# Kernel tuning notes

Hardware: AMD Instinct MI355X
Metric: run time of the kernel (lower is better)

Reference implementation:

```python
import jax, jax.numpy as jnp
from jax import lax
import numpy as np

REG = 0.1  # regularization_strength
EPS = 1e-12  # F.normalize clamp


def pav_nonincreasing(y):
    """Pool-Adjacent-Violators: argmin_v ||v - y||^2 s.t. v_1 >= v_2 >= ... >= v_n.
    Stack-based O(n) sweep, jit-compatible (fixed shapes)."""
    n = y.shape[0]
    sums0 = jnp.zeros(n, y.dtype)
    cnts0 = jnp.zeros(n, y.dtype)

    def body(i, state):
        sums, cnts, ptr = state
        cur_s = y[i]
        cur_c = jnp.asarray(1.0, y.dtype)

        def cond(c):
            cs, cc, p, sm, ct = c
            j = jnp.maximum(p - 1, 0)
            # merge while prev block mean < current mean (violates nonincreasing)
            return (p > 0) & (sm[j] * cc < cs * ct[j])

        def merge(c):
            cs, cc, p, sm, ct = c
            return (cs + sm[p - 1], cc + ct[p - 1], p - 1, sm, ct)

        cs, cc, p, sums, cnts = lax.while_loop(cond, merge, (cur_s, cur_c, ptr, sums, cnts))
        sums = sums.at[p].set(cs)
        cnts = cnts.at[p].set(cc)
        return (sums, cnts, p + 1)

    sums, cnts, ptr = lax.fori_loop(0, n, body, (sums0, cnts0, jnp.int32(0)))
    means = sums / jnp.maximum(cnts, 1)
    bounds = jnp.cumsum(cnts)  # block end positions; bounds[ptr-1] == n, stale tail harmless
    bid = jnp.searchsorted(bounds, jnp.arange(n, dtype=y.dtype) + 0.5)
    return means[bid]


def soft_rank_desc_row(values):
    """fast-soft-sort soft_rank, direction='DESCENDING', regularization='l2'.
    Projection of values*scale onto permutahedron(n..1) via isotonic regression."""
    n = values.shape[0]
    scale = -1.0 / REG  # DESCENDING => sign = -1
    z = values * scale
    perm = jnp.argsort(-z)           # sort z descending
    s = z[perm]
    w = jnp.arange(n, 0, -1, dtype=values.dtype)  # n, n-1, ..., 1
    dual = pav_nonincreasing(s - w)
    primal = s - dual
    inv = jnp.argsort(perm)
    return primal[inv]


def setup_inputs() -> dict:
    key = jax.random.key(0)
    kq, kc = jax.random.split(key)
    query_embed = jax.random.normal(kq, (16, 384), dtype=jnp.float32)
    corpus_embeds = jax.random.normal(kc, (50000, 384), dtype=jnp.float32)
    return {"query_embed": query_embed, "corpus_embeds": corpus_embeds, "k": 100}


def reference(query_embed, corpus_embeds, k):
    q = query_embed / jnp.maximum(
        jnp.linalg.norm(query_embed, axis=-1, keepdims=True), EPS)
    c = corpus_embeds / jnp.maximum(
        jnp.linalg.norm(corpus_embeds, axis=-1, keepdims=True), EPS)
    similarities = q @ c.T  # (batch, num_docs) cosine sims
    soft_ranks = jax.vmap(soft_rank_desc_row)(similarities)
    return similarities, soft_ranks
```

## Files before the change

### kernel.cpp

```cpp
#include <hip/hip_runtime.h>
#include <hip/hip_bf16.h>

#define NQ 16
#define DIM 384
#define KSTEPS (DIM / 32)
#define SUMS_STRIDE 16

typedef __attribute__((ext_vector_type(8))) short bf16x8;
typedef __attribute__((ext_vector_type(4))) float f32x4;

__global__ __launch_bounds__(128) void norm_q_kernel(
    const float* __restrict__ q, __hip_bfloat16* __restrict__ qbf,
    float* __restrict__ sums) {
  int b = blockIdx.x, t = threadIdx.x;
  float ss = 0.f;
  for (int k = t; k < DIM; k += 128) {
    float x = q[b * DIM + k];
    ss += x * x;
  }
  #pragma unroll
  for (int o = 32; o > 0; o >>= 1) ss += __shfl_down(ss, o, 64);
  __shared__ float wsum[2];
  if ((t & 63) == 0) wsum[t >> 6] = ss;
  __syncthreads();
  float inv = 1.0f / fmaxf(sqrtf(wsum[0] + wsum[1]), 1e-12f);
  for (int k = t; k < DIM; k += 128)
    qbf[b * DIM + k] = __float2bfloat16(q[b * DIM + k] * inv);
  if (b == 0 && t < NQ) sums[t * SUMS_STRIDE] = 0.f;
}

__global__ __launch_bounds__(256, 3) void sim_mfma_kernel(
    const float* __restrict__ corpus, const __hip_bfloat16* __restrict__ qbf,
    float* __restrict__ out_sims, float* __restrict__ sums, int n) {
  int lane = threadIdx.x & 63;
  int wid = threadIdx.x >> 6;
  int col = lane & 15;
  int quad = lane >> 4;
  int doc = blockIdx.x * 64 + wid * 16 + col;
  int dload = doc < n ? doc : n - 1;

  bf16x8 afrag[KSTEPS];
  const __hip_bfloat16* qrow = qbf + col * DIM + quad * 8;
  #pragma unroll
  for (int ks = 0; ks < KSTEPS; ++ks)
    afrag[ks] = *reinterpret_cast<const bf16x8*>(qrow + ks * 32);

  const float4* crow =
      reinterpret_cast<const float4*>(corpus + (size_t)dload * DIM + quad * 8);
  float4 v[2 * KSTEPS];
  #pragma unroll
  for (int ks = 0; ks < KSTEPS; ++ks) {
    v[2 * ks] = crow[ks * 8];
    v[2 * ks + 1] = crow[ks * 8 + 1];
  }

  f32x4 acc = {0.f, 0.f, 0.f, 0.f};
  float nrm2 = 0.f;
  #pragma unroll
  for (int ks = 0; ks < KSTEPS; ++ks) {
    float4 v0 = v[2 * ks], v1 = v[2 * ks + 1];
    nrm2 += v0.x * v0.x + v0.y * v0.y + v0.z * v0.z + v0.w * v0.w +
            v1.x * v1.x + v1.y * v1.y + v1.z * v1.z + v1.w * v1.w;
    union { bf16x8 b; __hip_bfloat162 h[4]; } u;
    u.h[0] = __float22bfloat162_rn(float2{v0.x, v0.y});
    u.h[1] = __float22bfloat162_rn(float2{v0.z, v0.w});
    u.h[2] = __float22bfloat162_rn(float2{v1.x, v1.y});
    u.h[3] = __float22bfloat162_rn(float2{v1.z, v1.w});
    acc = __builtin_amdgcn_mfma_f32_16x16x32_bf16(afrag[ks], u.b, acc, 0, 0, 0);
  }

  nrm2 += __shfl_xor(nrm2, 16, 64);
  nrm2 += __shfl_xor(nrm2, 32, 64);
  float inv = 1.0f / fmaxf(sqrtf(nrm2), 1e-12f);

  bool valid = doc < n;
  float vv[4];
  #pragma unroll
  for (int i = 0; i < 4; ++i) {
    float s = acc[i] * inv;
    if (valid) out_sims[(size_t)(quad * 4 + i) * n + doc] = s;
    float vr = valid ? s : 0.f;
    #pragma unroll
    for (int o = 1; o < 16; o <<= 1) vr += __shfl_xor(vr, o, 64);
    vv[i] = vr;
  }

  __shared__ float part[4][NQ];
  if (col == 0) {
    #pragma unroll
    for (int i = 0; i < 4; ++i) part[wid][quad * 4 + i] = vv[i];
  }
  __syncthreads();
  if (threadIdx.x < NQ) {
    float t = part[0][threadIdx.x] + part[1][threadIdx.x] +
              part[2][threadIdx.x] + part[3][threadIdx.x];
    atomicAdd(&sums[threadIdx.x * SUMS_STRIDE], t);
  }
}

__global__ __launch_bounds__(256) void rank4_kernel(
    const float4* __restrict__ sims4, const float* __restrict__ sums,
    float4* __restrict__ out4, int n4, float half_np1, float inv_n) {
  int b = blockIdx.y;
  int i = blockIdx.x * 256 + threadIdx.x;
  if (i >= n4) return;
  float base = 10.0f * sums[b * SUMS_STRIDE] * inv_n + half_np1;
  float4 v = sims4[(size_t)b * n4 + i];
  float4 r;
  r.x = base - 10.0f * v.x;
  r.y = base - 10.0f * v.y;
  r.z = base - 10.0f * v.z;
  r.w = base - 10.0f * v.w;
  out4[(size_t)b * n4 + i] = r;
}

__global__ __launch_bounds__(256) void rank1_kernel(
    const float* __restrict__ sims, const float* __restrict__ sums,
    float* __restrict__ out, int n, float half_np1, float inv_n) {
  int b = blockIdx.y;
  int i = blockIdx.x * 256 + threadIdx.x;
  if (i >= n) return;
  float base = 10.0f * sums[b * SUMS_STRIDE] * inv_n + half_np1;
  out[(size_t)b * n + i] = base - 10.0f * sims[(size_t)b * n + i];
}

extern "C" void kernel_launch(void* const* d_in, const int* in_sizes, int n_in,
                              void* d_out, int out_size, void* d_ws,
                              size_t ws_size, hipStream_t stream) {
  const float* q = (const float*)d_in[0];
  const float* corpus = (const float*)d_in[1];
  int n = in_sizes[1] / DIM;
  float* out = (float*)d_out;
  float* ranks = out + (size_t)NQ * n;

  float* ws_f = (float*)d_ws;
  float* sums = ws_f;
  __hip_bfloat16* qbf = (__hip_bfloat16*)(ws_f + NQ * SUMS_STRIDE);

  norm_q_kernel<<<NQ, 128, 0, stream>>>(q, qbf, sums);
  sim_mfma_kernel<<<(n + 63) / 64, 256, 0, stream>>>(corpus, qbf, out, sums, n);

  float half_np1 = 0.5f * (float)(n + 1);
  float inv_n = 1.0f / (float)n;
  if ((n & 3) == 0) {
    int n4 = n >> 2;
    dim3 g((n4 + 255) / 256, NQ);
    rank4_kernel<<<g, 256, 0, stream>>>((const float4*)out, sums,
                                        (float4*)ranks, n4, half_np1, inv_n);
  } else {
    dim3 g((n + 255) / 256, NQ);
    rank1_kernel<<<g, 256, 0, stream>>>(out, sums, ranks, n, half_np1, inv_n);
  }
}
```

Measured before the change: 130.7 us.

## Split K across waves per 16-doc block and bin atomic row sums

Each block now handles 16 documents and splits the 384-wide dot product across its 4 waves (split-K). Partial MFMA accumulators and squared norms are reduced through shared memory before wave 0 writes the similarities. The per-row sums used for the soft rank now go to 64 bins to reduce atomic contention, and the rank kernels fold those bins with a wave reduction. The aim is more parallelism, fewer registers per thread and higher occupancy. The cost is four times as many blocks plus the shared-memory reduction, and three of the four waves sit idle during the epilogue.

```diff
diff --git a/kernel.cpp b/kernel.cpp
--- a/kernel.cpp
+++ b/kernel.cpp
@@ -3,8 +3,7 @@
 
 #define NQ 16
 #define DIM 384
-#define KSTEPS (DIM / 32)
-#define SUMS_STRIDE 16
+#define NBINS 64
 
 typedef __attribute__((ext_vector_type(8))) short bf16x8;
 typedef __attribute__((ext_vector_type(4))) float f32x4;
@@ -26,39 +25,37 @@
   float inv = 1.0f / fmaxf(sqrtf(wsum[0] + wsum[1]), 1e-12f);
   for (int k = t; k < DIM; k += 128)
     qbf[b * DIM + k] = __float2bfloat16(q[b * DIM + k] * inv);
-  if (b == 0 && t < NQ) sums[t * SUMS_STRIDE] = 0.f;
+  if (t < NBINS) sums[b * NBINS + t] = 0.f;
 }
 
-__global__ __launch_bounds__(256, 3) void sim_mfma_kernel(
+__global__ __launch_bounds__(256, 6) void sim_mfma_kernel(
     const float* __restrict__ corpus, const __hip_bfloat16* __restrict__ qbf,
     float* __restrict__ out_sims, float* __restrict__ sums, int n) {
   int lane = threadIdx.x & 63;
-  int wid = threadIdx.x >> 6;
+  int w = threadIdx.x >> 6;
   int col = lane & 15;
   int quad = lane >> 4;
-  int doc = blockIdx.x * 64 + wid * 16 + col;
+  int doc = blockIdx.x * 16 + col;
   int dload = doc < n ? doc : n - 1;
 
-  bf16x8 afrag[KSTEPS];
+  const float* crow = corpus + (size_t)dload * DIM + quad * 8;
   const __hip_bfloat16* qrow = qbf + col * DIM + quad * 8;
+
+  float4 v[6];
   #pragma unroll
-  for (int ks = 0; ks < KSTEPS; ++ks)
-    afrag[ks] = *reinterpret_cast<const bf16x8*>(qrow + ks * 32);
-
-  const float4* crow =
-      reinterpret_cast<const float4*>(corpus + (size_t)dload * DIM + quad * 8);
-  float4 v[2 * KSTEPS];
-  #pragma unroll
-  for (int ks = 0; ks < KSTEPS; ++ks) {
-    v[2 * ks] = crow[ks * 8];
-    v[2 * ks + 1] = crow[ks * 8 + 1];
+  for (int s = 0; s < 3; ++s) {
+    int ks = w + 4 * s;
+    v[2 * s] = *reinterpret_cast<const float4*>(crow + ks * 32);
+    v[2 * s + 1] = *reinterpret_cast<const float4*>(crow + ks * 32 + 4);
   }
 
   f32x4 acc = {0.f, 0.f, 0.f, 0.f};
   float nrm2 = 0.f;
   #pragma unroll
-  for (int ks = 0; ks < KSTEPS; ++ks) {
-    float4 v0 = v[2 * ks], v1 = v[2 * ks + 1];
+  for (int s = 0; s < 3; ++s) {
+    int ks = w + 4 * s;
+    bf16x8 a = *reinterpret_cast<const bf16x8*>(qrow + ks * 32);
+    float4 v0 = v[2 * s], v1 = v[2 * s + 1];
     nrm2 += v0.x * v0.x + v0.y * v0.y + v0.z * v0.z + v0.w * v0.w +
             v1.x * v1.x + v1.y * v1.y + v1.z * v1.z + v1.w * v1.w;
     union { bf16x8 b; __hip_bfloat162 h[4]; } u;
@@ -66,35 +63,37 @@
     u.h[1] = __float22bfloat162_rn(float2{v0.z, v0.w});
     u.h[2] = __float22bfloat162_rn(float2{v1.x, v1.y});
     u.h[3] = __float22bfloat162_rn(float2{v1.z, v1.w});
-    acc = __builtin_amdgcn_mfma_f32_16x16x32_bf16(afrag[ks], u.b, acc, 0, 0, 0);
+    acc = __builtin_amdgcn_mfma_f32_16x16x32_bf16(a, u.b, acc, 0, 0, 0);
   }
 
-  nrm2 += __shfl_xor(nrm2, 16, 64);
-  nrm2 += __shfl_xor(nrm2, 32, 64);
-  float inv = 1.0f / fmaxf(sqrtf(nrm2), 1e-12f);
+  __shared__ float part[4][64 * 5];
+  float* myp = &part[w][lane * 5];
+  myp[0] = acc[0]; myp[1] = acc[1]; myp[2] = acc[2]; myp[3] = acc[3];
+  myp[4] = nrm2;
+  __syncthreads();
 
-  bool valid = doc < n;
-  float vv[4];
-  #pragma unroll
-  for (int i = 0; i < 4; ++i) {
-    float s = acc[i] * inv;
-    if (valid) out_sims[(size_t)(quad * 4 + i) * n + doc] = s;
-    float vr = valid ? s : 0.f;
+  if (w == 0) {
+    float a0 = 0.f, a1 = 0.f, a2 = 0.f, a3 = 0.f, nn = 0.f;
     #pragma unroll
-    for (int o = 1; o < 16; o <<= 1) vr += __shfl_xor(vr, o, 64);
-    vv[i] = vr;
-  }
+    for (int ww = 0; ww < 4; ++ww) {
+      const float* p = &part[ww][lane * 5];
+      a0 += p[0]; a1 += p[1]; a2 += p[2]; a3 += p[3]; nn += p[4];
+    }
+    nn += __shfl_xor(nn, 16, 64);
+    nn += __shfl_xor(nn, 32, 64);
+    float inv = 1.0f / fmaxf(sqrtf(nn), 1e-12f);
 
-  __shared__ float part[4][NQ];
-  if (col == 0) {
+    bool valid = doc < n;
+    float s4[4] = {a0 * inv, a1 * inv, a2 * inv, a3 * inv};
+    int bin = blockIdx.x & (NBINS - 1);
     #pragma unroll
-    for (int i = 0; i < 4; ++i) part[wid][quad * 4 + i] = vv[i];
-  }
-  __syncthreads();
-  if (threadIdx.x < NQ) {
-    float t = part[0][threadIdx.x] + part[1][threadIdx.x] +
-              part[2][threadIdx.x] + part[3][threadIdx.x];
-    atomicAdd(&sums[threadIdx.x * SUMS_STRIDE], t);
+    for (int i = 0; i < 4; ++i) {
+      if (valid) out_sims[(size_t)(quad * 4 + i) * n + doc] = s4[i];
+      float vr = valid ? s4[i] : 0.f;
+      #pragma unroll
+      for (int o = 1; o < 16; o <<= 1) vr += __shfl_xor(vr, o, 64);
+      if (col == 0) atomicAdd(&sums[(quad * 4 + i) * NBINS + bin], vr);
+    }
   }
 }
 
@@ -102,9 +101,12 @@
     const float4* __restrict__ sims4, const float* __restrict__ sums,
     float4* __restrict__ out4, int n4, float half_np1, float inv_n) {
   int b = blockIdx.y;
+  float bsum = sums[b * NBINS + (threadIdx.x & 63)];
+  #pragma unroll
+  for (int o = 32; o > 0; o >>= 1) bsum += __shfl_xor(bsum, o, 64);
   int i = blockIdx.x * 256 + threadIdx.x;
   if (i >= n4) return;
-  float base = 10.0f * sums[b * SUMS_STRIDE] * inv_n + half_np1;
+  float base = 10.0f * bsum * inv_n + half_np1;
   float4 v = sims4[(size_t)b * n4 + i];
   float4 r;
   r.x = base - 10.0f * v.x;
@@ -118,9 +120,12 @@
     const float* __restrict__ sims, const float* __restrict__ sums,
     float* __restrict__ out, int n, float half_np1, float inv_n) {
   int b = blockIdx.y;
+  float bsum = sums[b * NBINS + (threadIdx.x & 63)];
+  #pragma unroll
+  for (int o = 32; o > 0; o >>= 1) bsum += __shfl_xor(bsum, o, 64);
   int i = blockIdx.x * 256 + threadIdx.x;
   if (i >= n) return;
-  float base = 10.0f * sums[b * SUMS_STRIDE] * inv_n + half_np1;
+  float base = 10.0f * bsum * inv_n + half_np1;
   out[(size_t)b * n + i] = base - 10.0f * sims[(size_t)b * n + i];
 }
 
@@ -135,10 +140,10 @@
 
   float* ws_f = (float*)d_ws;
   float* sums = ws_f;
-  __hip_bfloat16* qbf = (__hip_bfloat16*)(ws_f + NQ * SUMS_STRIDE);
+  __hip_bfloat16* qbf = (__hip_bfloat16*)(ws_f + NQ * NBINS);
 
   norm_q_kernel<<<NQ, 128, 0, stream>>>(q, qbf, sums);
-  sim_mfma_kernel<<<(n + 63) / 64, 256, 0, stream>>>(corpus, qbf, out, sums, n);
+  sim_mfma_kernel<<<(n + 15) / 16, 256, 0, stream>>>(corpus, qbf, out, sums, n);
 
   float half_np1 = 0.5f * (float)(n + 1);
   float inv_n = 1.0f / (float)n;
```

New measurement: 125.0 us. 4.4% less time.
